# Optimization experiments

Measured on AMD Instinct MI355X. Metric: run time of the kernel, lower is better.

Reference implementation:

```python
import jax, jax.numpy as jnp
import numpy as np

N = 50000       # nodes
E = 1600000     # edges (avg degree 32)
IN = 64         # in_channels
ED = 16         # edge_dim
H = 128         # hidden_channels


def setup_inputs() -> dict:
    key = jax.random.key(0)
    ks = jax.random.split(key, 32)
    rn = lambda k, shape, s: jax.random.normal(k, shape, jnp.float32) * s
    inp = {}
    inp['x'] = rn(ks[0], (N, IN), 1.0)
    inp['edge_index'] = jax.random.randint(ks[1], (2, E), 0, N, dtype=jnp.int64)
    inp['edge_attr'] = rn(ks[2], (E, ED), 1.0)
    # per-layer params: edge linear (ED -> node_dim), MLP (d_in->H, H->H)
    node_dims = [IN, H, H]
    i = 3
    for l, d in enumerate(node_dims):
        inp[f'We{l}'] = rn(ks[i], (ED, d), 1.0 / np.sqrt(ED)); i += 1
        inp[f'be{l}'] = jnp.zeros((d,), jnp.float32)
        inp[f'W1_{l}'] = rn(ks[i], (d, H), 1.0 / np.sqrt(d)); i += 1
        inp[f'b1_{l}'] = jnp.zeros((H,), jnp.float32)
        inp[f'W2_{l}'] = rn(ks[i], (H, H), 1.0 / np.sqrt(H)); i += 1
        inp[f'b2_{l}'] = jnp.zeros((H,), jnp.float32)
    inp['Wlin'] = rn(ks[i], (H, 1), 1.0 / np.sqrt(H))
    inp['blin'] = jnp.zeros((1,), jnp.float32)
    return inp


def gine_conv(x, src, dst, ea, We, be, W1, b1, W2, b2):
    # message: relu(x_j + Lin_e(edge_attr)); aggregate: sum into dst; eps=0
    msg = jax.nn.relu(x[src] + ea @ We + be)            # [E, d]
    agg = jax.ops.segment_sum(msg, dst, num_segments=x.shape[0])  # [N, d]
    h = x + agg                                          # (1+eps)*x + agg, eps=0
    return jax.nn.relu(h @ W1 + b1) @ W2 + b2            # MLP


def reference(x, edge_index, edge_attr,
              We0, be0, W1_0, b1_0, W2_0, b2_0,
              We1, be1, W1_1, b1_1, W2_1, b2_1,
              We2, be2, W1_2, b1_2, W2_2, b2_2,
              Wlin, blin):
    src, dst = edge_index[0], edge_index[1]
    h = jax.nn.relu(gine_conv(x, src, dst, edge_attr, We0, be0, W1_0, b1_0, W2_0, b2_0))
    h = jax.nn.relu(gine_conv(h, src, dst, edge_attr, We1, be1, W1_1, b1_1, W2_1, b2_1))
    h = jax.nn.relu(gine_conv(h, src, dst, edge_attr, We2, be2, W1_2, b1_2, W2_2, b2_2))
    out = jax.nn.sigmoid(h @ Wlin + blin)                # [N, 1]
    return out.squeeze(-1)                               # [N]
```

## Files before the change

kernel.cpp:

```cpp
#include <hip/hip_runtime.h>
#include <math.h>


#define BLK 256

typedef __attribute__((ext_vector_type(2))) float f32x2;

__device__ inline f32x2 pk_fma(f32x2 a, f32x2 b, f32x2 c) {
    f32x2 d;
    asm("v_pk_fma_f32 %0, %1, %2, %3" : "=v"(d) : "v"(a), "v"(b), "v"(c));
    return d;
}


__global__ void detect_kernel(const unsigned int* __restrict__ ei, int* __restrict__ flag) {
    int t = blockIdx.x * blockDim.x + threadIdx.x;
    if (t < 1024) {
        if (ei[2 * t + 1] != 0u) atomicOr(flag, 1);
    }
}

__global__ void convert_hist_kernel(const int* __restrict__ ei32, const long long* __restrict__ ei64,
                                    const int* __restrict__ flag, int E,
                                    int* __restrict__ src, int* __restrict__ dst,
                                    int* __restrict__ counts) {
    int e = blockIdx.x * blockDim.x + threadIdx.x;
    if (e >= E) return;
    int s, d;
    if (*flag) { s = ei32[e]; d = ei32[E + e]; }
    else       { s = (int)ei64[e]; d = (int)ei64[E + e]; }
    src[e] = s; dst[e] = d;
    atomicAdd(&counts[d], 1);
}

__global__ void scan_kernel(const int* __restrict__ counts, int* __restrict__ offsets, int n) {
    __shared__ int tsum[256];
    __shared__ int texcl[256];
    int t = threadIdx.x;
    int chunk = (n + 255) >> 8;
    int b = t * chunk, e = min(b + chunk, n);
    int s = 0;
    for (int i = b; i < e; i++) s += counts[i];
    tsum[t] = s;
    __syncthreads();
    if (t == 0) {
        int run = 0;
        for (int i = 0; i < 256; i++) { texcl[i] = run; run += tsum[i]; }
        offsets[n] = run;
    }
    __syncthreads();
    int run = texcl[t];
    for (int i = b; i < e; i++) { offsets[i] = run; run += counts[i]; }
}

__global__ void scatter_pos_kernel(const int* __restrict__ src, const int* __restrict__ dst,
                                   const int* __restrict__ offsets, int* __restrict__ cursor,
                                   int2* __restrict__ meta, int E) {
    int e = blockIdx.x * blockDim.x + threadIdx.x;
    if (e >= E) return;
    int d = dst[e];
    int pos = offsets[d] + atomicAdd(&cursor[d], 1);
    meta[pos] = make_int2(src[e], e);
}

__global__ void permute_gather_kernel(const int2* __restrict__ meta,
                                      const float4* __restrict__ ea4,
                                      int* __restrict__ srcp, float4* __restrict__ eap4, int E) {
    int t = blockIdx.x * blockDim.x + threadIdx.x;
    if (t >= E * 4) return;
    int pos = t >> 2, c = t & 3;
    int2 m = meta[pos];
    eap4[(size_t)pos * 4 + c] = ea4[(size_t)m.y * 4 + c];
    if (c == 0) srcp[pos] = m.x;
}

template <int D>
__global__ __launch_bounds__(256) void aggregate_kernel(
    const float* __restrict__ x, const float* __restrict__ eap,
    const int* __restrict__ srcp,
    const float* __restrict__ We, const float* __restrict__ be,
    const int* __restrict__ offsets,
    float* __restrict__ h, int n) {
    constexpr int C = D / 64;
    int lane = threadIdx.x & 63;
    int node = __builtin_amdgcn_readfirstlane(blockIdx.x * 4 + (threadIdx.x >> 6));
    if (node >= n) return;
    int c0 = lane * C;

    f32x2 wp[C][8];
#pragma unroll
    for (int j = 0; j < C; j++)
#pragma unroll
        for (int t = 0; t < 8; t++) {
            f32x2 v; v.x = We[(2 * t) * D + c0 + j]; v.y = We[(2 * t + 1) * D + c0 + j];
            wp[j][t] = v;
        }
    float bias[C], acc[C];
#pragma unroll
    for (int j = 0; j < C; j++) {
        bias[j] = be[c0 + j];
        acc[j] = x[(size_t)node * D + c0 + j];
    }
    int p = offsets[node], pe = offsets[node + 1];

    for (; p + 8 <= pe; p += 8) {
        int s[8];
#pragma unroll
        for (int u = 0; u < 8; u++) s[u] = srcp[p + u];
        float xv[8][C];
#pragma unroll
        for (int u = 0; u < 8; u++) {
            const float* r = x + (size_t)s[u] * D + c0;
            if constexpr (C == 2) { float2 tv = *(const float2*)r; xv[u][0] = tv.x; xv[u][1] = tv.y; }
            else xv[u][0] = *r;
        }
#pragma unroll
        for (int u = 0; u < 8; u++) {
            const float4* er = (const float4*)(eap + (size_t)(p + u) * 16);
            float4 e0 = er[0], e1 = er[1], e2 = er[2], e3 = er[3];
            f32x2 ev[8];
            ev[0].x = e0.x; ev[0].y = e0.y;  ev[1].x = e0.z; ev[1].y = e0.w;
            ev[2].x = e1.x; ev[2].y = e1.y;  ev[3].x = e1.z; ev[3].y = e1.w;
            ev[4].x = e2.x; ev[4].y = e2.y;  ev[5].x = e2.z; ev[5].y = e2.w;
            ev[6].x = e3.x; ev[6].y = e3.y;  ev[7].x = e3.z; ev[7].y = e3.w;
#pragma unroll
            for (int j = 0; j < C; j++) {
                f32x2 prod; prod.x = xv[u][j] + bias[j]; prod.y = 0.f;
#pragma unroll
                for (int t = 0; t < 8; t++) prod = pk_fma(ev[t], wp[j][t], prod);
                acc[j] += fmaxf(prod.x + prod.y, 0.f);
            }
        }
    }
    for (; p < pe; p++) {
        int s = srcp[p];
        const float* xr = x + (size_t)s * D + c0;
        float xv[C];
        if constexpr (C == 2) { float2 t = *(const float2*)xr; xv[0] = t.x; xv[1] = t.y; }
        else xv[0] = *xr;
        const float4* er = (const float4*)(eap + (size_t)p * 16);
        float4 e0 = er[0], e1 = er[1], e2 = er[2], e3 = er[3];
        f32x2 ev[8];
        ev[0].x = e0.x; ev[0].y = e0.y;  ev[1].x = e0.z; ev[1].y = e0.w;
        ev[2].x = e1.x; ev[2].y = e1.y;  ev[3].x = e1.z; ev[3].y = e1.w;
        ev[4].x = e2.x; ev[4].y = e2.y;  ev[5].x = e2.z; ev[5].y = e2.w;
        ev[6].x = e3.x; ev[6].y = e3.y;  ev[7].x = e3.z; ev[7].y = e3.w;
#pragma unroll
        for (int j = 0; j < C; j++) {
            f32x2 prod; prod.x = xv[j] + bias[j]; prod.y = 0.f;
#pragma unroll
            for (int t = 0; t < 8; t++) prod = pk_fma(ev[t], wp[j][t], prod);
            acc[j] += fmaxf(prod.x + prod.y, 0.f);
        }
    }
#pragma unroll
    for (int j = 0; j < C; j++) h[(size_t)node * D + c0 + j] = acc[j];
}

template <int K>
__global__ __launch_bounds__(256) void mlp_kernel(
    const float* __restrict__ A, const float* __restrict__ W1, const float* __restrict__ b1,
    const float* __restrict__ W2, const float* __restrict__ b2,
    float* __restrict__ C, int n) {
    __shared__ __align__(16) float As[16][68];
    __shared__ __align__(16) float Bs[16][128];
    __shared__ __align__(16) float Ts[64][132];
    int t = threadIdx.x;
    int row0 = blockIdx.x * 64;
    int tr = t >> 5, tc = t & 31;
    float acc[8][4];
#pragma unroll
    for (int r = 0; r < 8; r++)
#pragma unroll
        for (int c = 0; c < 4; c++) acc[r][c] = 0.f;

    int lr = t >> 2, lk = (t & 3) * 4;
    int bk = t >> 4, bc = (t & 15) * 8;

    for (int ks = 0; ks < K; ks += 16) {
        float4 a;
        int grow = row0 + lr;
        if (grow < n) a = *(const float4*)(A + (size_t)grow * K + ks + lk);
        else a = make_float4(0.f, 0.f, 0.f, 0.f);
        As[lk + 0][lr] = a.x; As[lk + 1][lr] = a.y;
        As[lk + 2][lr] = a.z; As[lk + 3][lr] = a.w;

        const float4* bp = (const float4*)(W1 + (size_t)(ks + bk) * 128 + bc);
        float4 b0 = bp[0], b1v = bp[1];
        *(float4*)&Bs[bk][bc] = b0;
        *(float4*)&Bs[bk][bc + 4] = b1v;
        __syncthreads();
#pragma unroll
        for (int kk = 0; kk < 16; kk++) {
            float4 a0 = *(const float4*)&As[kk][tr * 8];
            float4 a1 = *(const float4*)&As[kk][tr * 8 + 4];
            float4 bv = *(const float4*)&Bs[kk][tc * 4];
            float ar[8] = {a0.x, a0.y, a0.z, a0.w, a1.x, a1.y, a1.z, a1.w};
            float bc4[4] = {bv.x, bv.y, bv.z, bv.w};
#pragma unroll
            for (int r = 0; r < 8; r++)
#pragma unroll
                for (int c = 0; c < 4; c++) acc[r][c] = fmaf(ar[r], bc4[c], acc[r][c]);
        }
        __syncthreads();
    }
    {
        float4 bb = *(const float4*)(b1 + tc * 4);
#pragma unroll
        for (int r = 0; r < 8; r++) {
            Ts[tr * 8 + r][tc * 4 + 0] = fmaxf(acc[r][0] + bb.x, 0.f);
            Ts[tr * 8 + r][tc * 4 + 1] = fmaxf(acc[r][1] + bb.y, 0.f);
            Ts[tr * 8 + r][tc * 4 + 2] = fmaxf(acc[r][2] + bb.z, 0.f);
            Ts[tr * 8 + r][tc * 4 + 3] = fmaxf(acc[r][3] + bb.w, 0.f);
        }
    }
    __syncthreads();

#pragma unroll
    for (int r = 0; r < 8; r++)
#pragma unroll
        for (int c = 0; c < 4; c++) acc[r][c] = 0.f;
    for (int ks = 0; ks < 128; ks += 16) {
        const float4* bp = (const float4*)(W2 + (size_t)(ks + bk) * 128 + bc);
        float4 b0 = bp[0], b1v = bp[1];
        *(float4*)&Bs[bk][bc] = b0;
        *(float4*)&Bs[bk][bc + 4] = b1v;
        __syncthreads();
#pragma unroll
        for (int kk = 0; kk < 16; kk++) {
            float4 bv = *(const float4*)&Bs[kk][tc * 4];
            float bc4[4] = {bv.x, bv.y, bv.z, bv.w};
            float ar[8];
#pragma unroll
            for (int r = 0; r < 8; r++) ar[r] = Ts[tr * 8 + r][ks + kk];
#pragma unroll
            for (int r = 0; r < 8; r++)
#pragma unroll
                for (int c = 0; c < 4; c++) acc[r][c] = fmaf(ar[r], bc4[c], acc[r][c]);
        }
        __syncthreads();
    }
    float4 bb = *(const float4*)(b2 + tc * 4);
#pragma unroll
    for (int r = 0; r < 8; r++) {
        int grow = row0 + tr * 8 + r;
        if (grow < n) {
            float4 v;
            v.x = fmaxf(acc[r][0] + bb.x, 0.f);
            v.y = fmaxf(acc[r][1] + bb.y, 0.f);
            v.z = fmaxf(acc[r][2] + bb.z, 0.f);
            v.w = fmaxf(acc[r][3] + bb.w, 0.f);
            *(float4*)(C + (size_t)grow * 128 + tc * 4) = v;
        }
    }
}

__global__ __launch_bounds__(256) void final_kernel(
    const float* __restrict__ x, const float* __restrict__ Wlin,
    const float* __restrict__ blin, float* __restrict__ out, int n) {
    int lane = threadIdx.x & 63;
    int node = blockIdx.x * 4 + (threadIdx.x >> 6);
    if (node >= n) return;
    float2 w = *(const float2*)(Wlin + lane * 2);
    float2 xv = *(const float2*)(x + (size_t)node * 128 + lane * 2);
    float v = xv.x * w.x + xv.y * w.y;
#pragma unroll
    for (int off = 32; off; off >>= 1) v += __shfl_down(v, off, 64);
    if (lane == 0) out[node] = 1.f / (1.f + expf(-(v + blin[0])));
}

extern "C" void kernel_launch(void* const* d_in, const int* in_sizes, int n_in,
                              void* d_out, int out_size, void* d_ws, size_t ws_size,
                              hipStream_t stream) {
    const float* x_in = (const float*)d_in[0];
    const void* ei    = d_in[1];
    const float* ea   = (const float*)d_in[2];
    const float* We[3]  = {(const float*)d_in[3], (const float*)d_in[9],  (const float*)d_in[15]};
    const float* be[3]  = {(const float*)d_in[4], (const float*)d_in[10], (const float*)d_in[16]};
    const float* W1[3]  = {(const float*)d_in[5], (const float*)d_in[11], (const float*)d_in[17]};
    const float* b1[3]  = {(const float*)d_in[6], (const float*)d_in[12], (const float*)d_in[18]};
    const float* W2[3]  = {(const float*)d_in[7], (const float*)d_in[13], (const float*)d_in[19]};
    const float* b2[3]  = {(const float*)d_in[8], (const float*)d_in[14], (const float*)d_in[20]};
    const float* Wlin = (const float*)d_in[21];
    const float* blin = (const float*)d_in[22];
    float* out = (float*)d_out;

    const int N = in_sizes[0] / 64;
    const int E = in_sizes[1] / 2;

    size_t off = 0;
    auto alloc = [&](size_t bytes) {
        void* p = (char*)d_ws + off;
        off += (bytes + 255) & ~(size_t)255;
        return p;
    };
    int*   flag    = (int*)alloc(4);
    int*   src32   = (int*)alloc((size_t)E * 4);
    int*   dst32   = (int*)alloc((size_t)E * 4);
    int*   counts  = (int*)alloc((size_t)N * 4);
    int*   offsets = (int*)alloc((size_t)(N + 1) * 4);
    int*   cursor  = (int*)alloc((size_t)N * 4);
    int2*  meta    = (int2*)alloc((size_t)E * 8);
    int*   srcp    = (int*)alloc((size_t)E * 4);
    float* eap     = (float*)alloc((size_t)E * 16 * 4);
    float* bufA    = (float*)alloc((size_t)N * 128 * 4);
    float* bufC    = (float*)alloc((size_t)N * 128 * 4);

    hipMemsetAsync(flag, 0, 4, stream);
    hipMemsetAsync(counts, 0, (size_t)N * 4, stream);
    hipMemsetAsync(cursor, 0, (size_t)N * 4, stream);

    int egrid = (E + BLK - 1) / BLK;
    detect_kernel<<<4, BLK, 0, stream>>>((const unsigned int*)ei, flag);
    convert_hist_kernel<<<egrid, BLK, 0, stream>>>((const int*)ei, (const long long*)ei, flag, E,
                                                   src32, dst32, counts);
    scan_kernel<<<1, BLK, 0, stream>>>(counts, offsets, N);
    scatter_pos_kernel<<<egrid, BLK, 0, stream>>>(src32, dst32, offsets, cursor, meta, E);
    permute_gather_kernel<<<(E * 4 + BLK - 1) / BLK, BLK, 0, stream>>>(
        meta, (const float4*)ea, srcp, (float4*)eap, E);

    int ngrid4 = (N + 3) / 4;
    int ggrid  = (N + 63) / 64;

    aggregate_kernel<64><<<ngrid4, BLK, 0, stream>>>(x_in, eap, srcp, We[0], be[0], offsets, bufA, N);
    mlp_kernel<64><<<ggrid, BLK, 0, stream>>>(bufA, W1[0], b1[0], W2[0], b2[0], bufC, N);
    aggregate_kernel<128><<<ngrid4, BLK, 0, stream>>>(bufC, eap, srcp, We[1], be[1], offsets, bufA, N);
    mlp_kernel<128><<<ggrid, BLK, 0, stream>>>(bufA, W1[1], b1[1], W2[1], b2[1], bufC, N);
    aggregate_kernel<128><<<ngrid4, BLK, 0, stream>>>(bufC, eap, srcp, We[2], be[2], offsets, bufA, N);
    mlp_kernel<128><<<ggrid, BLK, 0, stream>>>(bufA, W1[2], b1[2], W2[2], b2[2], bufC, N);

    final_kernel<<<ngrid4, BLK, 0, stream>>>(bufC, Wlin, blin, out, N);
}
```

Before: 1.040 ms.

## Scalar-load edge rows in aggregate, drop edge-index staging, fuse head into MLP

The aggregate kernel now loads each 16-float edge-attribute row as one wave-uniform vector and feeds it to v_pk_fma_f32 as a scalar (SGPR) operand, and its edge unroll drops from 8 to 4. The aim is to cut per-lane vector loads and VGPR pressure for data that is the same across the wave. Preprocessing no longer writes the intermediate src32/dst32 arrays; the histogram and scatter kernels read edge_index directly. The final linear and sigmoid head is folded into the last MLP kernel's epilogue via shuffles, which removes one launch and one full write and read of the hidden features. The risk is that the compiler may not keep the edge row in SGPRs, and the smaller unroll leaves fewer gathers in flight.

```diff
diff --git a/kernel.cpp b/kernel.cpp
--- a/kernel.cpp
+++ b/kernel.cpp
@@ -5,12 +5,18 @@
 #define BLK 256
 
 typedef __attribute__((ext_vector_type(2))) float f32x2;
-
-__device__ inline f32x2 pk_fma(f32x2 a, f32x2 b, f32x2 c) {
+typedef __attribute__((ext_vector_type(16))) float f32x16;
+
+__device__ inline f32x2 pk_fma_s(f32x2 a_uniform, f32x2 b, f32x2 c) {
     f32x2 d;
-    asm("v_pk_fma_f32 %0, %1, %2, %3" : "=v"(d) : "v"(a), "v"(b), "v"(c));
+    asm("v_pk_fma_f32 %0, %1, %2, %3" : "=v"(d) : "s"(a_uniform), "v"(b), "v"(c));
     return d;
 }
+
+union EdgeRow {
+    f32x16 v;
+    f32x2 p[8];
+};
 
 
 __global__ void detect_kernel(const unsigned int* __restrict__ ei, int* __restrict__ flag) {
@@ -20,16 +26,11 @@
     }
 }
 
-__global__ void convert_hist_kernel(const int* __restrict__ ei32, const long long* __restrict__ ei64,
-                                    const int* __restrict__ flag, int E,
-                                    int* __restrict__ src, int* __restrict__ dst,
-                                    int* __restrict__ counts) {
+__global__ void hist_kernel(const void* __restrict__ ei, const int* __restrict__ flag, int E,
+                            int* __restrict__ counts) {
     int e = blockIdx.x * blockDim.x + threadIdx.x;
     if (e >= E) return;
-    int s, d;
-    if (*flag) { s = ei32[e]; d = ei32[E + e]; }
-    else       { s = (int)ei64[e]; d = (int)ei64[E + e]; }
-    src[e] = s; dst[e] = d;
+    int d = (*flag) ? ((const int*)ei)[E + e] : (int)((const long long*)ei)[E + e];
     atomicAdd(&counts[d], 1);
 }
 
@@ -53,14 +54,16 @@
     for (int i = b; i < e; i++) { offsets[i] = run; run += counts[i]; }
 }
 
-__global__ void scatter_pos_kernel(const int* __restrict__ src, const int* __restrict__ dst,
+__global__ void scatter_pos_kernel(const void* __restrict__ ei, const int* __restrict__ flag,
                                    const int* __restrict__ offsets, int* __restrict__ cursor,
                                    int2* __restrict__ meta, int E) {
     int e = blockIdx.x * blockDim.x + threadIdx.x;
     if (e >= E) return;
-    int d = dst[e];
+    int s, d;
+    if (*flag) { s = ((const int*)ei)[e]; d = ((const int*)ei)[E + e]; }
+    else       { s = (int)((const long long*)ei)[e]; d = (int)((const long long*)ei)[E + e]; }
     int pos = offsets[d] + atomicAdd(&cursor[d], 1);
-    meta[pos] = make_int2(src[e], e);
+    meta[pos] = make_int2(s, e);
 }
 
 __global__ void permute_gather_kernel(const int2* __restrict__ meta,
@@ -103,31 +106,32 @@
     }
     int p = offsets[node], pe = offsets[node + 1];
 
-    for (; p + 8 <= pe; p += 8) {
-        int s[8];
-#pragma unroll
-        for (int u = 0; u < 8; u++) s[u] = srcp[p + u];
-        float xv[8][C];
-#pragma unroll
-        for (int u = 0; u < 8; u++) {
-            const float* r = x + (size_t)s[u] * D + c0;
-            if constexpr (C == 2) { float2 tv = *(const float2*)r; xv[u][0] = tv.x; xv[u][1] = tv.y; }
-            else xv[u][0] = *r;
-        }
-#pragma unroll
-        for (int u = 0; u < 8; u++) {
-            const float4* er = (const float4*)(eap + (size_t)(p + u) * 16);
-            float4 e0 = er[0], e1 = er[1], e2 = er[2], e3 = er[3];
-            f32x2 ev[8];
-            ev[0].x = e0.x; ev[0].y = e0.y;  ev[1].x = e0.z; ev[1].y = e0.w;
-            ev[2].x = e1.x; ev[2].y = e1.y;  ev[3].x = e1.z; ev[3].y = e1.w;
-            ev[4].x = e2.x; ev[4].y = e2.y;  ev[5].x = e2.z; ev[5].y = e2.w;
-            ev[6].x = e3.x; ev[6].y = e3.y;  ev[7].x = e3.z; ev[7].y = e3.w;
+    for (; p + 4 <= pe; p += 4) {
+        int s0 = srcp[p], s1 = srcp[p + 1], s2 = srcp[p + 2], s3 = srcp[p + 3];
+        float xv[4][C];
+        {
+            const float* r0 = x + (size_t)s0 * D + c0;
+            const float* r1 = x + (size_t)s1 * D + c0;
+            const float* r2 = x + (size_t)s2 * D + c0;
+            const float* r3 = x + (size_t)s3 * D + c0;
+            if constexpr (C == 2) {
+                float2 t0 = *(const float2*)r0, t1 = *(const float2*)r1;
+                float2 t2 = *(const float2*)r2, t3 = *(const float2*)r3;
+                xv[0][0] = t0.x; xv[0][1] = t0.y; xv[1][0] = t1.x; xv[1][1] = t1.y;
+                xv[2][0] = t2.x; xv[2][1] = t2.y; xv[3][0] = t3.x; xv[3][1] = t3.y;
+            } else {
+                xv[0][0] = *r0; xv[1][0] = *r1; xv[2][0] = *r2; xv[3][0] = *r3;
+            }
+        }
+#pragma unroll
+        for (int u = 0; u < 4; u++) {
+            EdgeRow er;
+            er.v = *(const f32x16*)(eap + (size_t)(p + u) * 16);
 #pragma unroll
             for (int j = 0; j < C; j++) {
                 f32x2 prod; prod.x = xv[u][j] + bias[j]; prod.y = 0.f;
 #pragma unroll
-                for (int t = 0; t < 8; t++) prod = pk_fma(ev[t], wp[j][t], prod);
+                for (int t = 0; t < 8; t++) prod = pk_fma_s(er.p[t], wp[j][t], prod);
                 acc[j] += fmaxf(prod.x + prod.y, 0.f);
             }
         }
@@ -138,18 +142,13 @@
         float xv[C];
         if constexpr (C == 2) { float2 t = *(const float2*)xr; xv[0] = t.x; xv[1] = t.y; }
         else xv[0] = *xr;
-        const float4* er = (const float4*)(eap + (size_t)p * 16);
-        float4 e0 = er[0], e1 = er[1], e2 = er[2], e3 = er[3];
-        f32x2 ev[8];
-        ev[0].x = e0.x; ev[0].y = e0.y;  ev[1].x = e0.z; ev[1].y = e0.w;
-        ev[2].x = e1.x; ev[2].y = e1.y;  ev[3].x = e1.z; ev[3].y = e1.w;
-        ev[4].x = e2.x; ev[4].y = e2.y;  ev[5].x = e2.z; ev[5].y = e2.w;
-        ev[6].x = e3.x; ev[6].y = e3.y;  ev[7].x = e3.z; ev[7].y = e3.w;
+        EdgeRow er;
+        er.v = *(const f32x16*)(eap + (size_t)p * 16);
 #pragma unroll
         for (int j = 0; j < C; j++) {
             f32x2 prod; prod.x = xv[j] + bias[j]; prod.y = 0.f;
 #pragma unroll
-            for (int t = 0; t < 8; t++) prod = pk_fma(ev[t], wp[j][t], prod);
+            for (int t = 0; t < 8; t++) prod = pk_fma_s(er.p[t], wp[j][t], prod);
             acc[j] += fmaxf(prod.x + prod.y, 0.f);
         }
     }
@@ -157,11 +156,12 @@
     for (int j = 0; j < C; j++) h[(size_t)node * D + c0 + j] = acc[j];
 }
 
-template <int K>
+template <int K, bool HEAD>
 __global__ __launch_bounds__(256) void mlp_kernel(
     const float* __restrict__ A, const float* __restrict__ W1, const float* __restrict__ b1,
     const float* __restrict__ W2, const float* __restrict__ b2,
-    float* __restrict__ C, int n) {
+    float* __restrict__ C, const float* __restrict__ Wlin, const float* __restrict__ blin,
+    float* __restrict__ out, int n) {
     __shared__ __align__(16) float As[16][68];
     __shared__ __align__(16) float Bs[16][128];
     __shared__ __align__(16) float Ts[64][132];
@@ -241,32 +241,35 @@
         __syncthreads();
     }
     float4 bb = *(const float4*)(b2 + tc * 4);
-#pragma unroll
-    for (int r = 0; r < 8; r++) {
-        int grow = row0 + tr * 8 + r;
-        if (grow < n) {
-            float4 v;
-            v.x = fmaxf(acc[r][0] + bb.x, 0.f);
-            v.y = fmaxf(acc[r][1] + bb.y, 0.f);
-            v.z = fmaxf(acc[r][2] + bb.z, 0.f);
-            v.w = fmaxf(acc[r][3] + bb.w, 0.f);
-            *(float4*)(C + (size_t)grow * 128 + tc * 4) = v;
-        }
-    }
-}
-
-__global__ __launch_bounds__(256) void final_kernel(
-    const float* __restrict__ x, const float* __restrict__ Wlin,
-    const float* __restrict__ blin, float* __restrict__ out, int n) {
-    int lane = threadIdx.x & 63;
-    int node = blockIdx.x * 4 + (threadIdx.x >> 6);
-    if (node >= n) return;
-    float2 w = *(const float2*)(Wlin + lane * 2);
-    float2 xv = *(const float2*)(x + (size_t)node * 128 + lane * 2);
-    float v = xv.x * w.x + xv.y * w.y;
-#pragma unroll
-    for (int off = 32; off; off >>= 1) v += __shfl_down(v, off, 64);
-    if (lane == 0) out[node] = 1.f / (1.f + expf(-(v + blin[0])));
+    if constexpr (HEAD) {
+        float4 wl = *(const float4*)(Wlin + tc * 4);
+        float bl = *blin;
+#pragma unroll
+        for (int r = 0; r < 8; r++) {
+            float v0 = fmaxf(acc[r][0] + bb.x, 0.f);
+            float v1 = fmaxf(acc[r][1] + bb.y, 0.f);
+            float v2 = fmaxf(acc[r][2] + bb.z, 0.f);
+            float v3 = fmaxf(acc[r][3] + bb.w, 0.f);
+            float part = v0 * wl.x + v1 * wl.y + v2 * wl.z + v3 * wl.w;
+#pragma unroll
+            for (int m = 1; m <= 16; m <<= 1) part += __shfl_xor(part, m, 64);
+            int grow = row0 + tr * 8 + r;
+            if (tc == 0 && grow < n) out[grow] = 1.f / (1.f + expf(-(part + bl)));
+        }
+    } else {
+#pragma unroll
+        for (int r = 0; r < 8; r++) {
+            int grow = row0 + tr * 8 + r;
+            if (grow < n) {
+                float4 v;
+                v.x = fmaxf(acc[r][0] + bb.x, 0.f);
+                v.y = fmaxf(acc[r][1] + bb.y, 0.f);
+                v.z = fmaxf(acc[r][2] + bb.z, 0.f);
+                v.w = fmaxf(acc[r][3] + bb.w, 0.f);
+                *(float4*)(C + (size_t)grow * 128 + tc * 4) = v;
+            }
+        }
+    }
 }
 
 extern "C" void kernel_launch(void* const* d_in, const int* in_sizes, int n_in,
@@ -295,8 +298,6 @@
         return p;
     };
     int*   flag    = (int*)alloc(4);
-    int*   src32   = (int*)alloc((size_t)E * 4);
-    int*   dst32   = (int*)alloc((size_t)E * 4);
     int*   counts  = (int*)alloc((size_t)N * 4);
     int*   offsets = (int*)alloc((size_t)(N + 1) * 4);
     int*   cursor  = (int*)alloc((size_t)N * 4);
@@ -306,16 +307,15 @@
     float* bufA    = (float*)alloc((size_t)N * 128 * 4);
     float* bufC    = (float*)alloc((size_t)N * 128 * 4);
 
-    hipMemsetAsync(flag, 0, 4, stream);
-    hipMemsetAsync(counts, 0, (size_t)N * 4, stream);
-    hipMemsetAsync(cursor, 0, (size_t)N * 4, stream);
+    (void)hipMemsetAsync(flag, 0, 4, stream);
+    (void)hipMemsetAsync(counts, 0, (size_t)N * 4, stream);
+    (void)hipMemsetAsync(cursor, 0, (size_t)N * 4, stream);
 
     int egrid = (E + BLK - 1) / BLK;
     detect_kernel<<<4, BLK, 0, stream>>>((const unsigned int*)ei, flag);
-    convert_hist_kernel<<<egrid, BLK, 0, stream>>>((const int*)ei, (const long long*)ei, flag, E,
-                                                   src32, dst32, counts);
+    hist_kernel<<<egrid, BLK, 0, stream>>>(ei, flag, E, counts);
     scan_kernel<<<1, BLK, 0, stream>>>(counts, offsets, N);
-    scatter_pos_kernel<<<egrid, BLK, 0, stream>>>(src32, dst32, offsets, cursor, meta, E);
+    scatter_pos_kernel<<<egrid, BLK, 0, stream>>>(ei, flag, offsets, cursor, meta, E);
     permute_gather_kernel<<<(E * 4 + BLK - 1) / BLK, BLK, 0, stream>>>(
         meta, (const float4*)ea, srcp, (float4*)eap, E);
 
@@ -323,11 +323,12 @@
     int ggrid  = (N + 63) / 64;
 
     aggregate_kernel<64><<<ngrid4, BLK, 0, stream>>>(x_in, eap, srcp, We[0], be[0], offsets, bufA, N);
-    mlp_kernel<64><<<ggrid, BLK, 0, stream>>>(bufA, W1[0], b1[0], W2[0], b2[0], bufC, N);
+    mlp_kernel<64, false><<<ggrid, BLK, 0, stream>>>(bufA, W1[0], b1[0], W2[0], b2[0], bufC,
+                                                     nullptr, nullptr, nullptr, N);
     aggregate_kernel<128><<<ngrid4, BLK, 0, stream>>>(bufC, eap, srcp, We[1], be[1], offsets, bufA, N);
-    mlp_kernel<128><<<ggrid, BLK, 0, stream>>>(bufA, W1[1], b1[1], W2[1], b2[1], bufC, N);
+    mlp_kernel<128, false><<<ggrid, BLK, 0, stream>>>(bufA, W1[1], b1[1], W2[1], b2[1], bufC,
+                                                      nullptr, nullptr, nullptr, N);
     aggregate_kernel<128><<<ngrid4, BLK, 0, stream>>>(bufC, eap, srcp, We[2], be[2], offsets, bufA, N);
-    mlp_kernel<128><<<ggrid, BLK, 0, stream>>>(bufA, W1[2], b1[2], W2[2], b2[2], bufC, N);
-
-    final_kernel<<<ngrid4, BLK, 0, stream>>>(bufC, Wlin, blin, out, N);
-}
+    mlp_kernel<128, true><<<ggrid, BLK, 0, stream>>>(bufA, W1[2], b1[2], W2[2], b2[2], nullptr,
+                                                     Wlin, blin, out, N);
+}
```

Measured after the change: 996.3 us. 1.04x faster.
